# Optimization experiments

Hardware: AMD Instinct MI355X
Metric: run time of the kernel (lower is better)

The kernel has to match this reference:

```python
import jax, jax.numpy as jnp
import numpy as np

IN_CH = 512
MID = max(IN_CH // 8, 1)


def setup_inputs() -> dict:
    key = jax.random.key(0)
    ks = jax.random.split(key, 8)
    B, C, H, W = 4, IN_CH, 64, 64
    s = 0.05
    x = jax.random.normal(ks[0], (B, C, H, W), dtype=jnp.float32)
    wq = jax.random.normal(ks[1], (MID, C), dtype=jnp.float32) * s
    bq = jnp.zeros((MID,), dtype=jnp.float32)
    wk = jax.random.normal(ks[2], (MID, C), dtype=jnp.float32) * s
    bk = jnp.zeros((MID,), dtype=jnp.float32)
    wv = jax.random.normal(ks[3], (C, C), dtype=jnp.float32) * s
    bv = jnp.zeros((C,), dtype=jnp.float32)
    alpha = jnp.ones((1,), dtype=jnp.float32) * 0.5  # nonzero so attention path is exercised
    return {"x": x, "wq": wq, "bq": bq, "wk": wk, "bk": bk, "wv": wv, "bv": bv, "alpha": alpha}


def reference(x, wq, bq, wk, bk, wv, bv, alpha):
    B, C, H, W = x.shape
    N = H * W
    xf = x.reshape(B, C, N)  # [B, C, N]
    # 1x1 convs == per-position channel GEMMs
    q = jnp.einsum('mc,bcn->bnm', wq, xf) + bq  # [B, N, mid]
    k = jnp.einsum('mc,bcn->bmn', wk, xf) + bk[None, :, None]  # [B, mid, N]
    v = jnp.einsum('dc,bcn->bdn', wv, xf) + bv[None, :, None]  # [B, C, N]
    attn = jax.nn.softmax(jnp.einsum('bnm,bmk->bnk', q, k), axis=-1)  # [B, N, N]
    out = jnp.einsum('bdn,bkn->bdk', v, attn)  # v @ attn^T -> [B, C, N]
    out = out.reshape(B, C, H, W)
    return alpha * out + x
```

## Files before the change

kernel.cpp:

```cpp
#include <hip/hip_runtime.h>

#define BB 4
#define CD 512
#define NP 4096
#define MID 64
#define PSTR 88

typedef _Float16 half8 __attribute__((ext_vector_type(8)));
typedef _Float16 half4 __attribute__((ext_vector_type(4)));
typedef float floatx4 __attribute__((ext_vector_type(4)));

#define LOG2E 1.4426950408889634f

__global__ __launch_bounds__(256) void prep_w(
    const float* __restrict__ wq, const float* __restrict__ wk,
    const float* __restrict__ wv, const float* __restrict__ bq,
    const float* __restrict__ bk, const float* __restrict__ bv,
    _Float16* __restrict__ w_h, float* __restrict__ bias) {
  int idx = blockIdx.x * 256 + threadIdx.x;
  for (int i = idx; i < 640 * 512; i += gridDim.x * 256) {
    int r = i >> 9, c = i & 511;
    float v = (r < 64) ? wq[(r << 9) + c] * LOG2E
            : (r < 128) ? wk[((r - 64) << 9) + c]
                        : wv[((r - 128) << 9) + c];
    w_h[i] = (_Float16)v;
  }
  if (idx < 640) {
    float v = (idx < 64) ? bq[idx] * LOG2E
            : (idx < 128) ? bk[idx - 64]
                          : bv[idx - 128];
    bias[idx] = v;
  }
}

__global__ __launch_bounds__(256) void transpose_x(const float* __restrict__ x,
                                                   _Float16* __restrict__ xt) {
  __shared__ float tile[64][65];
  int b = blockIdx.z, c0 = blockIdx.y * 64, n0 = blockIdx.x * 64;
  int t = threadIdx.x;
  const float* xb = x + (size_t)b * CD * NP;
#pragma unroll
  for (int k = 0; k < 16; k++) {
    int cl = k * 4 + (t >> 6);
    int nl = t & 63;
    tile[cl][nl] = xb[(size_t)(c0 + cl) * NP + n0 + nl];
  }
  __syncthreads();
  _Float16* xtb = xt + ((size_t)b * NP + n0) * CD + c0;
#pragma unroll
  for (int k = 0; k < 2; k++) {
    int nl = k * 32 + (t >> 3);
    int cl = (t & 7) * 8;
    half8 pk;
#pragma unroll
    for (int i = 0; i < 8; i++) pk[i] = (_Float16)tile[cl + i][nl];
    *(half8*)(xtb + (size_t)nl * CD + cl) = pk;
  }
}

__global__ __launch_bounds__(256, 2) void proj_qkv(
    const _Float16* __restrict__ w_h, const float* __restrict__ bias,
    const _Float16* __restrict__ xt, _Float16* __restrict__ q_h,
    _Float16* __restrict__ k_h, _Float16* __restrict__ v_h) {
  __shared__ _Float16 xls[64 * 512];
  int t = threadIdx.x, w = t >> 6, lane = t & 63;
  int col = lane & 15, quad = lane >> 4;
  int rbh = blockIdx.x, nb = blockIdx.y, b = blockIdx.z;
  int n0 = nb * 64;
  const _Float16* xtb = xt + ((size_t)b * NP + n0) * CD;

#pragma unroll
  for (int j = 0; j < 16; j++) {
    int u = t + j * 256;
    int row = u >> 6, un = u & 63;
    *(half8*)(xls + row * 512 + ((un ^ (row & 7)) << 3)) =
        *(const half8*)(xtb + (size_t)row * CD + un * 8);
  }
  __syncthreads();

  int rw = rbh * 320 + w * 80;
  floatx4 acc[5][4] = {};
  for (int c = 0; c < CD; c += 32) {
    int cu = c >> 3;
    half8 a[5], bf[4];
#pragma unroll
    for (int i = 0; i < 5; i++)
      a[i] = *(const half8*)(w_h + (size_t)(rw + i * 16 + col) * CD + c + quad * 8);
#pragma unroll
    for (int j = 0; j < 4; j++) {
      int row = j * 16 + col;
      bf[j] = *(const half8*)(xls + row * 512 + (((cu + quad) ^ (row & 7)) << 3));
    }
#pragma unroll
    for (int i = 0; i < 5; i++)
#pragma unroll
      for (int j = 0; j < 4; j++)
        acc[i][j] = __builtin_amdgcn_mfma_f32_16x16x32_f16(a[i], bf[j], acc[i][j], 0, 0, 0);
  }

#pragma unroll
  for (int i = 0; i < 5; i++) {
    int r0 = rw + i * 16;
    float bi[4];
#pragma unroll
    for (int rr = 0; rr < 4; rr++) bi[rr] = bias[r0 + quad * 4 + rr];
    if (r0 < 128) {
      _Float16* dst = (r0 < 64 ? q_h + (size_t)b * NP * MID + r0
                               : k_h + (size_t)b * NP * MID + (r0 - 64));
#pragma unroll
      for (int j = 0; j < 4; j++) {
        int n = n0 + j * 16 + col;
        half4 pk;
#pragma unroll
        for (int rr = 0; rr < 4; rr++) pk[rr] = (_Float16)(acc[i][j][rr] + bi[rr]);
        *(half4*)(dst + (size_t)n * MID + quad * 4) = pk;
      }
    } else {
      int dbase = r0 - 128 + quad * 4;
#pragma unroll
      for (int j = 0; j < 4; j++) {
        int n = n0 + j * 16 + col;
#pragma unroll
        for (int rr = 0; rr < 4; rr++)
          v_h[((size_t)b * CD + dbase + rr) * NP + n] =
              (_Float16)(acc[i][j][rr] + bi[rr]);
      }
    }
  }
}

__global__ __launch_bounds__(256) void rowmax(const _Float16* __restrict__ q_h,
                                              const _Float16* __restrict__ k_h,
                                              float* __restrict__ M) {
  int qb = blockIdx.x, b = blockIdx.y;
  int t = threadIdx.x, w = t >> 6, lane = t & 63;
  int col = lane & 15, quad = lane >> 4;
  int q0 = qb * 32;
  const _Float16* qp = q_h + ((size_t)b * NP + q0) * MID;
  half8 bq[2][2];
#pragma unroll
  for (int qt = 0; qt < 2; qt++)
#pragma unroll
    for (int h = 0; h < 2; h++)
      bq[qt][h] = *(const half8*)(qp + (size_t)(qt * 16 + col) * MID + h * 32 + quad * 8);
  const _Float16* kp = k_h + ((size_t)b * NP + (size_t)w * 1024) * MID;
  float m[2] = {-1e30f, -1e30f};
#pragma unroll 4
  for (int n = 0; n < 1024; n += 16) {
    half8 ak0 = *(const half8*)(kp + (size_t)(n + col) * MID + quad * 8);
    half8 ak1 = *(const half8*)(kp + (size_t)(n + col) * MID + 32 + quad * 8);
#pragma unroll
    for (int qt = 0; qt < 2; qt++) {
      floatx4 s = {};
      s = __builtin_amdgcn_mfma_f32_16x16x32_f16(ak0, bq[qt][0], s, 0, 0, 0);
      s = __builtin_amdgcn_mfma_f32_16x16x32_f16(ak1, bq[qt][1], s, 0, 0, 0);
      m[qt] = fmaxf(m[qt], fmaxf(fmaxf(s[0], s[1]), fmaxf(s[2], s[3])));
    }
  }
  __shared__ float red[4][2][16];
#pragma unroll
  for (int qt = 0; qt < 2; qt++) {
    m[qt] = fmaxf(m[qt], __shfl_xor(m[qt], 16));
    m[qt] = fmaxf(m[qt], __shfl_xor(m[qt], 32));
  }
  if (quad == 0) {
    red[w][0][col] = m[0];
    red[w][1][col] = m[1];
  }
  __syncthreads();
  if (t < 32) {
    int qt = t >> 4, c = t & 15;
    float mm = fmaxf(fmaxf(red[0][qt][c], red[1][qt][c]),
                     fmaxf(red[2][qt][c], red[3][qt][c]));
    M[(size_t)b * NP + q0 + t] = mm;
  }
}

__global__ __launch_bounds__(256, 2) void attn_pv(
    const _Float16* __restrict__ q_h, const _Float16* __restrict__ k_h,
    const _Float16* __restrict__ v_h, const float* __restrict__ M,
    const float* __restrict__ x, const float* __restrict__ alpha_p,
    float* __restrict__ out) {
  int bid = blockIdx.x;
  int combo = bid & 7;
  int b = combo >> 1, ds = combo & 1;
  int qb = bid >> 3;
  int q0 = qb * 64, d0 = ds * 256;

  int t = threadIdx.x, w = t >> 6, lane = t & 63;
  int col = lane & 15, quad = lane >> 4;

  __shared__ _Float16 pbuf[2][64 * PSTR];
  __shared__ float lred[4][4][16];
  __shared__ float lfin[64];

  const _Float16* qp = q_h + ((size_t)b * NP + q0) * MID;
  half8 bq[4][2];
#pragma unroll
  for (int qt = 0; qt < 4; qt++)
#pragma unroll
    for (int h = 0; h < 2; h++)
      bq[qt][h] = *(const half8*)(qp + (size_t)(qt * 16 + col) * MID + h * 32 + quad * 8);
  float Mq[4];
#pragma unroll
  for (int qt = 0; qt < 4; qt++) Mq[qt] = M[(size_t)b * NP + q0 + qt * 16 + col];

  const _Float16* kp = k_h + (size_t)b * NP * MID;
  const _Float16* vp = v_h + ((size_t)(b * CD + d0) + w * 64) * NP;

  floatx4 acc[4][4] = {};
  float lp[4] = {0.f, 0.f, 0.f, 0.f};

  for (int ci = 0; ci < 64; ci++) {
    int nc = ci * 64;
    _Float16* pb = pbuf[ci & 1];

    const _Float16* kr = kp + (size_t)(nc + w * 16 + col) * MID;
    half8 ak0 = *(const half8*)(kr + quad * 8);
    half8 ak1 = *(const half8*)(kr + 32 + quad * 8);

    half8 av[2][4];
#pragma unroll
    for (int f = 0; f < 2; f++)
#pragma unroll
      for (int dt = 0; dt < 4; dt++)
        av[f][dt] = *(const half8*)(vp + (size_t)(dt * 16 + col) * NP + nc + f * 32 + quad * 8);

#pragma unroll
    for (int qt = 0; qt < 4; qt++) {
      floatx4 s = {};
      s = __builtin_amdgcn_mfma_f32_16x16x32_f16(ak0, bq[qt][0], s, 0, 0, 0);
      s = __builtin_amdgcn_mfma_f32_16x16x32_f16(ak1, bq[qt][1], s, 0, 0, 0);
      half4 pk;
#pragma unroll
      for (int r = 0; r < 4; r++) {
        float p = exp2f(s[r] - Mq[qt]);
        lp[qt] += p;
        pk[r] = (_Float16)p;
      }
      *(half4*)(pb + (qt * 16 + col) * PSTR + w * 16 + quad * 4) = pk;
    }
    __syncthreads();

#pragma unroll
    for (int f = 0; f < 2; f++) {
      half8 bp[4];
#pragma unroll
      for (int qt = 0; qt < 4; qt++)
        bp[qt] = *(const half8*)(pb + (qt * 16 + col) * PSTR + f * 32 + quad * 8);
#pragma unroll
      for (int dt = 0; dt < 4; dt++)
#pragma unroll
        for (int qt = 0; qt < 4; qt++)
          acc[dt][qt] = __builtin_amdgcn_mfma_f32_16x16x32_f16(av[f][dt], bp[qt], acc[dt][qt], 0, 0, 0);
    }
  }

#pragma unroll
  for (int qt = 0; qt < 4; qt++) {
    lp[qt] += __shfl_xor(lp[qt], 16);
    lp[qt] += __shfl_xor(lp[qt], 32);
    if (quad == 0) lred[w][qt][col] = lp[qt];
  }
  __syncthreads();
  if (t < 64) {
    int qt = t >> 4, c = t & 15;
    float l = lred[0][qt][c] + lred[1][qt][c] + lred[2][qt][c] + lred[3][qt][c];
    lfin[t] = alpha_p[0] / l;
  }
  __syncthreads();

  const float* xp = x + ((size_t)(b * CD + d0) + w * 64) * NP;
  float* op = out + ((size_t)(b * CD + d0) + w * 64) * NP;
#pragma unroll
  for (int dt = 0; dt < 4; dt++)
#pragma unroll
    for (int qt = 0; qt < 4; qt++) {
      float linv = lfin[qt * 16 + col];
#pragma unroll
      for (int r = 0; r < 4; r++) {
        size_t o = (size_t)(dt * 16 + quad * 4 + r) * NP + q0 + qt * 16 + col;
        op[o] = acc[dt][qt][r] * linv + xp[o];
      }
    }
}

extern "C" void kernel_launch(void* const* d_in, const int* in_sizes, int n_in,
                              void* d_out, int out_size, void* d_ws, size_t ws_size,
                              hipStream_t stream) {
  const float* x     = (const float*)d_in[0];
  const float* wq    = (const float*)d_in[1];
  const float* bq    = (const float*)d_in[2];
  const float* wk    = (const float*)d_in[3];
  const float* bk    = (const float*)d_in[4];
  const float* wv    = (const float*)d_in[5];
  const float* bv    = (const float*)d_in[6];
  const float* alpha = (const float*)d_in[7];
  float* out = (float*)d_out;

  char* ws = (char*)d_ws;
  _Float16* w_h  = (_Float16*)(ws);
  float*    bias = (float*)(ws + 655360);
  float*    Mbuf = (float*)(ws + 657920);
  _Float16* xt   = (_Float16*)(ws + 723456);
  _Float16* q_h  = (_Float16*)(ws + 17500672);
  _Float16* k_h  = (_Float16*)(ws + 19597824);
  _Float16* v_h  = (_Float16*)(ws + 21694976);

  prep_w<<<1280, 256, 0, stream>>>(wq, wk, wv, bq, bk, bv, w_h, bias);
  transpose_x<<<dim3(64, 8, BB), 256, 0, stream>>>(x, xt);
  proj_qkv<<<dim3(2, 64, BB), 256, 0, stream>>>(w_h, bias, xt, q_h, k_h, v_h);
  rowmax<<<dim3(128, BB), 256, 0, stream>>>(q_h, k_h, Mbuf);
  attn_pv<<<512, 256, 0, stream>>>(q_h, k_h, v_h, Mbuf, x, alpha, out);
}
```

Measured before the change: 308.1 us.

## Stage K and V tiles through LDS with async global_load_lds double buffering

Replaces per-thread register loads of K and V in the attention-PV loop with asynchronous global-to-LDS DMA (global_load_lds_dwordx4). The next chunk's K and V are prefetched into double-buffered swizzled LDS while the current chunk is computed, and the P tile reuses the K buffer region. It also uses the hardware exp2 builtin and raises wave priority around the MFMA block. The aim is to hide global memory latency behind MFMA work. In exchange it relies on hand-tuned vmcnt/lgkmcnt waits and raw barriers that are fragile, and the final-iteration prefetch wraps to chunk 0, which is wasted traffic.

```diff
diff --git a/kernel.cpp b/kernel.cpp
--- a/kernel.cpp
+++ b/kernel.cpp
@@ -4,7 +4,6 @@
 #define CD 512
 #define NP 4096
 #define MID 64
-#define PSTR 88
 
 typedef _Float16 half8 __attribute__((ext_vector_type(8)));
 typedef _Float16 half4 __attribute__((ext_vector_type(4)));
@@ -68,7 +67,6 @@
   int rbh = blockIdx.x, nb = blockIdx.y, b = blockIdx.z;
   int n0 = nb * 64;
   const _Float16* xtb = xt + ((size_t)b * NP + n0) * CD;
-
 #pragma unroll
   for (int j = 0; j < 16; j++) {
     int u = t + j * 256;
@@ -175,6 +173,13 @@
     M[(size_t)b * NP + q0 + t] = mm;
   }
 }
+
+#define DMA16(gp, ldsoff)                                                      \
+  asm volatile("s_mov_b32 m0, %0\n\t"                                         \
+               "global_load_lds_dwordx4 %1, off"                              \
+               :: "s"(__builtin_amdgcn_readfirstlane((int)(ldsoff))),          \
+                  "v"(gp)                                                      \
+               : "memory")
 
 __global__ __launch_bounds__(256, 2) void attn_pv(
     const _Float16* __restrict__ q_h, const _Float16* __restrict__ k_h,
@@ -189,10 +194,14 @@
 
   int t = threadIdx.x, w = t >> 6, lane = t & 63;
   int col = lane & 15, quad = lane >> 4;
-
-  __shared__ _Float16 pbuf[2][64 * PSTR];
-  __shared__ float lred[4][4][16];
-  __shared__ float lfin[64];
+  int c7 = col & 7;
+
+  __shared__ floatx4 smem4[50432 / 16];
+  char* smem = (char*)smem4;
+  char* vbufB = smem;
+  char* kbufB = smem + 32768;
+  float* lred = (float*)(smem + 49152);
+  float* lfin = (float*)(smem + 50176);
 
   const _Float16* qp = q_h + ((size_t)b * NP + q0) * MID;
   half8 bq[4][2];
@@ -205,27 +214,45 @@
 #pragma unroll
   for (int qt = 0; qt < 4; qt++) Mq[qt] = M[(size_t)b * NP + q0 + qt * 16 + col];
 
-  const _Float16* kp = k_h + (size_t)b * NP * MID;
-  const _Float16* vp = v_h + ((size_t)(b * CD + d0) + w * 64) * NP;
+  int klane = (lane >> 3) * MID + (((lane & 7) ^ ((lane >> 3) & 7)) << 3);
+  size_t vlane = (size_t)(lane >> 2) * NP + ((lane & 3) << 3);
+
+  const _Float16* kgb = k_h + (size_t)b * NP * MID;
+  const _Float16* vgb = v_h + (size_t)(b * CD + d0 + w * 64) * NP;
 
   floatx4 acc[4][4] = {};
   float lp[4] = {0.f, 0.f, 0.f, 0.f};
 
+  int kdw = 32768 + w * 2048;
+  int vdw = w * 4096;
+
+#pragma unroll
+  for (int j = 0; j < 2; j++)
+    DMA16(kgb + (size_t)(0 + w * 16 + j * 8) * MID + klane, kdw + j * 1024);
+#pragma unroll
+  for (int h = 0; h < 2; h++)
+#pragma unroll
+    for (int j = 0; j < 4; j++)
+      DMA16(vgb + (size_t)(j * 16) * NP + h * 32 + vlane,
+            h * 16384 + vdw + j * 1024);
+
   for (int ci = 0; ci < 64; ci++) {
-    int nc = ci * 64;
-    _Float16* pb = pbuf[ci & 1];
-
-    const _Float16* kr = kp + (size_t)(nc + w * 16 + col) * MID;
-    half8 ak0 = *(const half8*)(kr + quad * 8);
-    half8 ak1 = *(const half8*)(kr + 32 + quad * 8);
-
-    half8 av[2][4];
-#pragma unroll
-    for (int f = 0; f < 2; f++)
-#pragma unroll
-      for (int dt = 0; dt < 4; dt++)
-        av[f][dt] = *(const half8*)(vp + (size_t)(dt * 16 + col) * NP + nc + f * 32 + quad * 8);
-
+    int p = ci & 1;
+    int nxt = ((ci + 1) & 63) * 64;
+
+    asm volatile("s_waitcnt lgkmcnt(0)\n\ts_barrier" ::: "memory");
+#pragma unroll
+    for (int j = 0; j < 2; j++)
+      DMA16(kgb + (size_t)(nxt + w * 16 + j * 8) * MID + klane,
+            kdw + (1 - p) * 8192 + j * 1024);
+
+    asm volatile("s_waitcnt vmcnt(10)" ::: "memory");
+
+    const char* kb = kbufB + p * 8192 + w * 2048;
+    int sl0 = quad ^ c7;
+    half8 ak0 = *(const half8*)(kb + col * 128 + (sl0 << 4));
+    half8 ak1 = *(const half8*)(kb + col * 128 + ((sl0 ^ 4) << 4));
+    char* pbW = kbufB + p * 8192;
 #pragma unroll
     for (int qt = 0; qt < 4; qt++) {
       floatx4 s = {};
@@ -234,25 +261,39 @@
       half4 pk;
 #pragma unroll
       for (int r = 0; r < 4; r++) {
-        float p = exp2f(s[r] - Mq[qt]);
-        lp[qt] += p;
-        pk[r] = (_Float16)p;
+        float pv = __builtin_amdgcn_exp2f(s[r] - Mq[qt]);
+        lp[qt] += pv;
+        pk[r] = (_Float16)pv;
       }
-      *(half4*)(pb + (qt * 16 + col) * PSTR + w * 16 + quad * 4) = pk;
-    }
-    __syncthreads();
-
-#pragma unroll
-    for (int f = 0; f < 2; f++) {
+      *(half4*)(pbW + w * 2048 + (qt * 16 + col) * 32 + quad * 8) = pk;
+    }
+
+    asm volatile("s_waitcnt lgkmcnt(0)\n\ts_barrier" ::: "memory");
+
+#pragma unroll
+    for (int h = 0; h < 2; h++) {
+      asm volatile("s_waitcnt vmcnt(6)" ::: "memory");
       half8 bp[4];
 #pragma unroll
       for (int qt = 0; qt < 4; qt++)
-        bp[qt] = *(const half8*)(pb + (qt * 16 + col) * PSTR + f * 32 + quad * 8);
+        bp[qt] = *(const half8*)(pbW + (2 * h + (quad >> 1)) * 2048 +
+                                 (qt * 16 + col) * 32 + ((quad & 1) << 4));
+      const char* vb = vbufB + h * 16384 + vdw;
+      half8 av[4];
 #pragma unroll
       for (int dt = 0; dt < 4; dt++)
+        av[dt] = *(const half8*)(vb + (dt * 16 + col) * 64 + (quad << 4));
+      __builtin_amdgcn_s_setprio(1);
+#pragma unroll
+      for (int dt = 0; dt < 4; dt++)
 #pragma unroll
         for (int qt = 0; qt < 4; qt++)
-          acc[dt][qt] = __builtin_amdgcn_mfma_f32_16x16x32_f16(av[f][dt], bp[qt], acc[dt][qt], 0, 0, 0);
+          acc[dt][qt] = __builtin_amdgcn_mfma_f32_16x16x32_f16(av[dt], bp[qt], acc[dt][qt], 0, 0, 0);
+      __builtin_amdgcn_s_setprio(0);
+#pragma unroll
+      for (int j = 0; j < 4; j++)
+        DMA16(vgb + (size_t)(j * 16) * NP + nxt + h * 32 + vlane,
+              h * 16384 + vdw + j * 1024);
     }
   }
 
@@ -260,12 +301,13 @@
   for (int qt = 0; qt < 4; qt++) {
     lp[qt] += __shfl_xor(lp[qt], 16);
     lp[qt] += __shfl_xor(lp[qt], 32);
-    if (quad == 0) lred[w][qt][col] = lp[qt];
+    if (quad == 0) lred[(w * 4 + qt) * 16 + col] = lp[qt];
   }
   __syncthreads();
   if (t < 64) {
     int qt = t >> 4, c = t & 15;
-    float l = lred[0][qt][c] + lred[1][qt][c] + lred[2][qt][c] + lred[3][qt][c];
+    float l = lred[(0 + qt) * 16 + c] + lred[(4 + qt) * 16 + c] +
+              lred[(8 + qt) * 16 + c] + lred[(12 + qt) * 16 + c];
     lfin[t] = alpha_p[0] / l;
   }
   __syncthreads();
```

After: 254.8 us. 1.21x faster.
